# Performance work log

Hardware: AMD Instinct MI355X
Metric: run time of the kernel (lower is better)

Reference implementation:

```python
import jax, jax.numpy as jnp
import numpy as np

N, E, EL = 65536, 1048576, 2097152
IN, H, OUT = 32, 64, 64


def setup_inputs() -> dict:
    key = jax.random.key(0)
    ks = jax.random.split(key, 20)
    inp = {
        "x": jax.random.normal(ks[0], (N, IN), dtype=jnp.float32),
        "edge_index": jax.random.randint(ks[1], (2, E), 0, N, dtype=jnp.int64),
        "edge_weight": jax.random.uniform(ks[2], (E,), dtype=jnp.float32),
        "edge_label_index": jax.random.randint(ks[3], (2, EL), 0, N, dtype=jnp.int64),
    }
    dims = [(IN, H), (H, H), (H, H), (H, H), (H, H), (H, OUT)]
    for i, (di, do) in enumerate(dims):
        scale = (2.0 / (di + do)) ** 0.5
        inp[f"w{i+1}"] = jax.random.normal(ks[4 + i], (di, do), dtype=jnp.float32) * scale
        inp[f"b{i+1}"] = jnp.zeros((do,), dtype=jnp.float32)
    return inp


def _gcn_norm(edge_index, edge_weight, num_nodes):
    # PyG GCNConv default: add self-loops (weight 1), symmetric normalization
    src, dst = edge_index[0], edge_index[1]
    loop = jnp.arange(num_nodes, dtype=edge_index.dtype)
    src_f = jnp.concatenate([src, loop])
    dst_f = jnp.concatenate([dst, loop])
    w_f = jnp.concatenate([edge_weight, jnp.ones((num_nodes,), edge_weight.dtype)])
    deg = jax.ops.segment_sum(w_f, dst_f, num_segments=num_nodes)
    dinv = jnp.where(deg > 0, jax.lax.rsqrt(jnp.where(deg > 0, deg, 1.0)), 0.0)
    norm = dinv[src_f] * w_f * dinv[dst_f]  # [E+N]
    return src_f, dst_f, norm


def _gcn_layer(x, W, b, src_f, dst_f, norm, num_nodes):
    h = x @ W  # transform first, then propagate (PyG GCNConv order)
    msg = norm[:, None] * h[src_f]  # gather + scale along edges
    out = jax.ops.segment_sum(msg, dst_f, num_segments=num_nodes)  # scatter-add
    return out + b


def reference(x, edge_index, edge_weight, edge_label_index,
              w1, b1, w2, b2, w3, b3, w4, b4, w5, b5, w6, b6):
    num_nodes = x.shape[0]
    src_f, dst_f, norm = _gcn_norm(edge_index, edge_weight, num_nodes)
    h = x
    for W, b in [(w1, b1), (w2, b2), (w3, b3), (w4, b4), (w5, b5)]:
        h = jax.nn.relu(_gcn_layer(h, W, b, src_f, dst_f, norm, num_nodes))
        # dropout = identity in deterministic reference
    encoded = _gcn_layer(h, w6, b6, src_f, dst_f, norm, num_nodes)
    # decode: elementwise dot over labeled edge pairs
    decoded = (encoded[edge_label_index[0]] * encoded[edge_label_index[1]]).sum(axis=1)
    return decoded
```

## Files before the change

kernel.cpp:

```cpp
#include <hip/hip_runtime.h>
#include <hip/hip_fp16.h>

#define N_NODES 65536
#define N_EDGES 1048576
#define N_LABEL 2097152
#define DIM_IN 32
#define DIM_H 64

typedef short short8 __attribute__((ext_vector_type(8)));
typedef float floatx4 __attribute__((ext_vector_type(4)));


__global__ void k_init(float* __restrict__ deg, int* __restrict__ cnt) {
    int v = blockIdx.x * blockDim.x + threadIdx.x;
    deg[v] = 1.0f;
    cnt[v] = 0;
}

__global__ void k_cnt(const int* __restrict__ ei, const float* __restrict__ w,
                      int* __restrict__ cnt, float* __restrict__ deg) {
    int e = blockIdx.x * blockDim.x + threadIdx.x;
    int d = ei[N_EDGES + e];
    atomicAdd(&cnt[d], 1);
    atomicAdd(&deg[d], w[e]);
}

__global__ void k_scan1(const int* __restrict__ cnt, int* __restrict__ blksum) {
    int tid = threadIdx.x;
    const int4* p = (const int4*)(cnt + blockIdx.x * 1024);
    int4 v = p[tid];
    int s = v.x + v.y + v.z + v.w;
    for (int d = 1; d < 64; d <<= 1) s += __shfl_xor(s, d);
    __shared__ int wsum[4];
    if ((tid & 63) == 0) wsum[tid >> 6] = s;
    __syncthreads();
    if (tid == 0) blksum[blockIdx.x] = wsum[0] + wsum[1] + wsum[2] + wsum[3];
}

__global__ void k_scan2(int* __restrict__ blksum) {
    if (threadIdx.x == 0) {
        int run = 0;
        for (int i = 0; i < 64; ++i) { int t = blksum[i]; blksum[i] = run; run += t; }
    }
}

__global__ void k_scan3(const int* __restrict__ cnt, const int* __restrict__ blksum,
                        int* __restrict__ offs, int* __restrict__ cursor) {
    int tid = threadIdx.x, bid = blockIdx.x;
    const int4* p = (const int4*)(cnt + bid * 1024);
    int4 v = p[tid];
    int s = v.x + v.y + v.z + v.w;
    int lane = tid & 63, wid = tid >> 6;
    int sc = s;
    for (int d = 1; d < 64; d <<= 1) {
        int t = __shfl_up(sc, d);
        if (lane >= d) sc += t;
    }
    __shared__ int wsum[4];
    if (lane == 63) wsum[wid] = sc;
    __syncthreads();
    int base = blksum[bid];
    for (int w2 = 0; w2 < wid; ++w2) base += wsum[w2];
    int ex = base + sc - s;
    int idx = bid * 1024 + tid * 4;
    int o0 = ex, o1 = o0 + v.x, o2 = o1 + v.y, o3 = o2 + v.z;
    offs[idx] = o0; offs[idx + 1] = o1; offs[idx + 2] = o2; offs[idx + 3] = o3;
    cursor[idx] = o0; cursor[idx + 1] = o1; cursor[idx + 2] = o2; cursor[idx + 3] = o3;
    if (bid == 63 && tid == 255) offs[N_NODES] = o3 + v.w;
}

__global__ void k_dinv(float* __restrict__ deg) {
    int v = blockIdx.x * blockDim.x + threadIdx.x;
    deg[v] = rsqrtf(deg[v]);
}

__global__ void k_fill(const int* __restrict__ ei, const float* __restrict__ w,
                       const float* __restrict__ dinv, int* __restrict__ cursor,
                       int2* __restrict__ csr_se) {
    int e = blockIdx.x * blockDim.x + threadIdx.x;
    int s = ei[e];
    int d = ei[N_EDGES + e];
    int pos = atomicAdd(&cursor[d], 1);
    float nm = dinv[s] * w[e] * dinv[d];
    csr_se[pos] = make_int2(s, __float_as_int(nm));
}


__global__ void k_cast_x(const float* __restrict__ x, __half* __restrict__ xh) {
    int gid = blockIdx.x * 256 + threadIdx.x;
    xh[gid] = __float2half(x[gid]);
}


template <int K>
__global__ void __launch_bounds__(256) k_agg(
        const int* __restrict__ offs, const int2* __restrict__ csr_se,
        const __half* __restrict__ h, const float* __restrict__ dinv,
        float* __restrict__ agg) {
    constexpr int LPE = K / 8;
    constexpr int EPI = 64 / LPE;

    int tid = threadIdx.x;
    int v = blockIdx.x * 4 + (tid >> 6);
    int lane = tid & 63;
    int sub = lane % LPE;
    int g   = lane / LPE;

    float a[8] = {0.f, 0.f, 0.f, 0.f, 0.f, 0.f, 0.f, 0.f};

    if (g == 0) {
        float dv = dinv[v];
        float sl = dv * dv;
        uint4 rv = *(const uint4*)(h + (size_t)v * K + sub * 8);
        const __half2* hp = (const __half2*)&rv;
#pragma unroll
        for (int i = 0; i < 4; ++i) {
            float2 f = __half22float2(hp[i]);
            a[2 * i]     += sl * f.x;
            a[2 * i + 1] += sl * f.y;
        }
    }

    int j0 = __builtin_amdgcn_readfirstlane(offs[v]);
    int j1 = __builtin_amdgcn_readfirstlane(offs[v + 1]);

    for (int jm = j0; jm < j1; jm += 64) {
        int mi = jm + lane;
        int2 md = csr_se[mi < j1 ? mi : j1 - 1];
        if (mi >= j1) md.y = 0;
        int nwin = j1 - jm;
        if (nwin > 64) nwin = 64;
        for (int t = 0; t * EPI < nwin; ++t) {
            int we = t * EPI + g;
            int src = __shfl(md.x, we);
            float nm = __int_as_float(__shfl(md.y, we));
            uint4 rv = *(const uint4*)(h + (size_t)src * K + sub * 8);
            const __half2* hp = (const __half2*)&rv;
#pragma unroll
            for (int i = 0; i < 4; ++i) {
                float2 f = __half22float2(hp[i]);
                a[2 * i]     += nm * f.x;
                a[2 * i + 1] += nm * f.y;
            }
        }
    }

#pragma unroll
    for (int st = LPE; st < 64; st <<= 1) {
#pragma unroll
        for (int i = 0; i < 8; ++i) a[i] += __shfl_xor(a[i], st);
    }

    if (lane < LPE) {
        float* dst = agg + (size_t)v * K + lane * 8;
        *(float4*)(dst)     = make_float4(a[0], a[1], a[2], a[3]);
        *(float4*)(dst + 4) = make_float4(a[4], a[5], a[6], a[7]);
    }
}


__device__ __forceinline__ unsigned short f32_bf16(float f) {
    unsigned u = __float_as_uint(f);
    unsigned r = u + 0x7FFFu + ((u >> 16) & 1u);
    return (unsigned short)(r >> 16);
}
__device__ __forceinline__ float bf16_f32(unsigned short h) {
    return __uint_as_float(((unsigned)h) << 16);
}

template <int KIN, bool RELU>
__global__ void __launch_bounds__(256) k_gemm_mfma(
        const float* __restrict__ agg, const float* __restrict__ W,
        const float* __restrict__ b, __half* __restrict__ out) {
    constexpr int KC = KIN / 32;
    constexpr int NT = N_NODES / 16;
    __shared__ float Wl[KIN * 64];
    int tid = threadIdx.x;
    for (int i = tid; i < KIN * 64; i += 256) Wl[i] = W[i];
    __syncthreads();

    int lane = tid & 63;
    int l15 = lane & 15, l4 = lane >> 4;

    short8 whi[4][KC], wlo[4][KC];
#pragma unroll
    for (int ct = 0; ct < 4; ++ct)
#pragma unroll
        for (int kc = 0; kc < KC; ++kc)
#pragma unroll
            for (int j = 0; j < 8; ++j) {
                float wv = Wl[(kc * 32 + l4 * 8 + j) * 64 + ct * 16 + l15];
                unsigned short hi = f32_bf16(wv);
                unsigned short lo = f32_bf16(wv - bf16_f32(hi));
                whi[ct][kc][j] = (short)hi;
                wlo[ct][kc][j] = (short)lo;
            }
    float bias[4];
#pragma unroll
    for (int ct = 0; ct < 4; ++ct) bias[ct] = b[ct * 16 + l15];

    int wave_id = blockIdx.x * 4 + (tid >> 6);
    for (int tile = wave_id; tile < NT; tile += 2048) {
        int r0 = tile * 16;
        const float* arow = agg + (size_t)(r0 + l15) * KIN + l4 * 8;
        short8 ahi[KC], alo[KC];
#pragma unroll
        for (int kc = 0; kc < KC; ++kc) {
            float4 f0 = *(const float4*)(arow + kc * 32);
            float4 f1 = *(const float4*)(arow + kc * 32 + 4);
            float fv[8] = {f0.x, f0.y, f0.z, f0.w, f1.x, f1.y, f1.z, f1.w};
#pragma unroll
            for (int j = 0; j < 8; ++j) {
                unsigned short hi = f32_bf16(fv[j]);
                unsigned short lo = f32_bf16(fv[j] - bf16_f32(hi));
                ahi[kc][j] = (short)hi;
                alo[kc][j] = (short)lo;
            }
        }
        floatx4 acc[4] = {{0.f,0.f,0.f,0.f},{0.f,0.f,0.f,0.f},{0.f,0.f,0.f,0.f},{0.f,0.f,0.f,0.f}};
#pragma unroll
        for (int ct = 0; ct < 4; ++ct)
#pragma unroll
            for (int kc = 0; kc < KC; ++kc) {
                acc[ct] = __builtin_amdgcn_mfma_f32_16x16x32_bf16(ahi[kc], whi[ct][kc], acc[ct], 0, 0, 0);
                acc[ct] = __builtin_amdgcn_mfma_f32_16x16x32_bf16(ahi[kc], wlo[ct][kc], acc[ct], 0, 0, 0);
                acc[ct] = __builtin_amdgcn_mfma_f32_16x16x32_bf16(alo[kc], whi[ct][kc], acc[ct], 0, 0, 0);
            }
#pragma unroll
        for (int ct = 0; ct < 4; ++ct)
#pragma unroll
            for (int r = 0; r < 4; ++r) {
                float o = acc[ct][r] + bias[ct];
                if (RELU) o = fmaxf(o, 0.f);
                out[(size_t)(r0 + l4 * 4 + r) * 64 + ct * 16 + l15] = __float2half(o);
            }
    }
}


__device__ __forceinline__ float dot8h(uint4 ua, uint4 ub) {
    const __half2* pa = (const __half2*)&ua;
    const __half2* pb = (const __half2*)&ub;
    float s = 0.f;
#pragma unroll
    for (int i = 0; i < 4; ++i) {
        float2 fa = __half22float2(pa[i]);
        float2 fb = __half22float2(pb[i]);
        s += fa.x * fb.x + fa.y * fb.y;
    }
    return s;
}

__global__ void __launch_bounds__(256) k_decode(
        const int* __restrict__ eli, const __half* __restrict__ enc,
        float* __restrict__ out) {
    int gid = blockIdx.x * 256 + threadIdx.x;
    int p = gid >> 3;
    int c8 = gid & 7;
    int a = eli[p];
    int b = eli[N_LABEL + p];
    uint4 ua = *(const uint4*)(enc + (size_t)a * 64 + c8 * 8);
    uint4 ub = *(const uint4*)(enc + (size_t)b * 64 + c8 * 8);
    float s = dot8h(ua, ub);
    s += __shfl_xor(s, 1, 8);
    s += __shfl_xor(s, 2, 8);
    s += __shfl_xor(s, 4, 8);
    if (c8 == 0) out[p] = s;
}


extern "C" void kernel_launch(void* const* d_in, const int* in_sizes, int n_in,
                              void* d_out, int out_size, void* d_ws, size_t ws_size,
                              hipStream_t stream) {
    const float* x   = (const float*)d_in[0];
    const int*   ei  = (const int*)d_in[1];
    const float* ew  = (const float*)d_in[2];
    const int*   eli = (const int*)d_in[3];
    const float* W[6] = {(const float*)d_in[4],  (const float*)d_in[6],
                         (const float*)d_in[8],  (const float*)d_in[10],
                         (const float*)d_in[12], (const float*)d_in[14]};
    const float* B[6] = {(const float*)d_in[5],  (const float*)d_in[7],
                         (const float*)d_in[9],  (const float*)d_in[11],
                         (const float*)d_in[13], (const float*)d_in[15]};

    char* ws = (char*)d_ws;
    float*  dinv    = (float*)ws;   ws += N_NODES * 4;
    int*    cnt     = (int*)ws;     ws += N_NODES * 4;
    int*    offs    = (int*)ws;     ws += (N_NODES + 16) * 4;
    int*    cursor  = (int*)ws;     ws += N_NODES * 4;
    int*    blksum  = (int*)ws;     ws += 256 * 4;
    int2*   csr_se  = (int2*)ws;    ws += (size_t)N_EDGES * 8;
    __half* xh      = (__half*)ws;  ws += (size_t)N_NODES * DIM_IN * 2;
    float*  aggF    = (float*)ws;   ws += (size_t)N_NODES * 64 * 4;
    __half* hA      = (__half*)ws;  ws += (size_t)N_NODES * 64 * 2;
    __half* hB      = (__half*)ws;

    const int BS = 256;
    const int gAgg = N_NODES / 4;
    const int gGemm = 512;

    k_init <<<N_NODES / BS, BS, 0, stream>>>(dinv, cnt);
    k_cnt  <<<N_EDGES / BS, BS, 0, stream>>>(ei, ew, cnt, dinv);
    k_scan1<<<64, BS, 0, stream>>>(cnt, blksum);
    k_scan2<<<1, 64, 0, stream>>>(blksum);
    k_scan3<<<64, BS, 0, stream>>>(cnt, blksum, offs, cursor);
    k_dinv <<<N_NODES / BS, BS, 0, stream>>>(dinv);
    k_fill <<<N_EDGES / BS, BS, 0, stream>>>(ei, ew, dinv, cursor, csr_se);

    k_cast_x<<<N_NODES * DIM_IN / BS, BS, 0, stream>>>(x, xh);

    k_agg<DIM_IN><<<gAgg, BS, 0, stream>>>(offs, csr_se, xh, dinv, aggF);
    k_gemm_mfma<DIM_IN, true><<<gGemm, BS, 0, stream>>>(aggF, W[0], B[0], hA);

    k_agg<DIM_H><<<gAgg, BS, 0, stream>>>(offs, csr_se, hA, dinv, aggF);
    k_gemm_mfma<DIM_H, true><<<gGemm, BS, 0, stream>>>(aggF, W[1], B[1], hB);
    k_agg<DIM_H><<<gAgg, BS, 0, stream>>>(offs, csr_se, hB, dinv, aggF);
    k_gemm_mfma<DIM_H, true><<<gGemm, BS, 0, stream>>>(aggF, W[2], B[2], hA);
    k_agg<DIM_H><<<gAgg, BS, 0, stream>>>(offs, csr_se, hA, dinv, aggF);
    k_gemm_mfma<DIM_H, true><<<gGemm, BS, 0, stream>>>(aggF, W[3], B[3], hB);
    k_agg<DIM_H><<<gAgg, BS, 0, stream>>>(offs, csr_se, hB, dinv, aggF);
    k_gemm_mfma<DIM_H, true><<<gGemm, BS, 0, stream>>>(aggF, W[4], B[4], hA);

    k_agg<DIM_H><<<gAgg, BS, 0, stream>>>(offs, csr_se, hA, dinv, aggF);
    k_gemm_mfma<DIM_H, false><<<gGemm, BS, 0, stream>>>(aggF, W[5], B[5], hB);

    k_decode<<<N_LABEL * 8 / BS, BS, 0, stream>>>(eli, hB, (float*)d_out);
}
```

Before: 490.1 us.

## Pack degree and count into one 64-bit atomic and record per-edge rank

The separate count and float-degree atomics are merged into a single 64-bit atomicAdd: the count sits in the high word and a 2^24 fixed-point weight sum in the low word. The returned old count is stored as each edge's rank, so the CSR fill computes its position as offs[d]+rank[e] and no longer needs a cursor array or a second round of atomics. This halves the atomic traffic in the degree pass and removes atomics from the fill pass. In exchange it adds a 16-bit rank array, makes the degree a fixed-point sum with small rounding error, and relies on per-node degree staying below 65536 and the weight sum fitting in 32 bits.

```diff
diff --git a/kernel.cpp b/kernel.cpp
--- a/kernel.cpp
+++ b/kernel.cpp
@@ -11,25 +11,25 @@
 typedef float floatx4 __attribute__((ext_vector_type(4)));
 
 
-__global__ void k_init(float* __restrict__ deg, int* __restrict__ cnt) {
+__global__ void k_init(unsigned long long* __restrict__ packed) {
     int v = blockIdx.x * blockDim.x + threadIdx.x;
-    deg[v] = 1.0f;
-    cnt[v] = 0;
+    packed[v] = 0ull;
 }
 
 __global__ void k_cnt(const int* __restrict__ ei, const float* __restrict__ w,
-                      int* __restrict__ cnt, float* __restrict__ deg) {
+                      unsigned long long* __restrict__ packed,
+                      unsigned short* __restrict__ rank) {
     int e = blockIdx.x * blockDim.x + threadIdx.x;
     int d = ei[N_EDGES + e];
-    atomicAdd(&cnt[d], 1);
-    atomicAdd(&deg[d], w[e]);
-}
-
-__global__ void k_scan1(const int* __restrict__ cnt, int* __restrict__ blksum) {
+    unsigned fx = __float2uint_rn(w[e] * 16777216.f);
+    unsigned long long old = atomicAdd(&packed[d], (1ull << 32) | (unsigned long long)fx);
+    rank[e] = (unsigned short)(old >> 32);
+}
+
+__global__ void k_scan1(const int2* __restrict__ packed, int* __restrict__ blksum) {
     int tid = threadIdx.x;
-    const int4* p = (const int4*)(cnt + blockIdx.x * 1024);
-    int4 v = p[tid];
-    int s = v.x + v.y + v.z + v.w;
+    const int2* p = packed + blockIdx.x * 1024 + tid * 4;
+    int s = p[0].y + p[1].y + p[2].y + p[3].y;
     for (int d = 1; d < 64; d <<= 1) s += __shfl_xor(s, d);
     __shared__ int wsum[4];
     if ((tid & 63) == 0) wsum[tid >> 6] = s;
@@ -44,12 +44,12 @@
     }
 }
 
-__global__ void k_scan3(const int* __restrict__ cnt, const int* __restrict__ blksum,
-                        int* __restrict__ offs, int* __restrict__ cursor) {
+__global__ void k_scan3(const int2* __restrict__ packed, const int* __restrict__ blksum,
+                        int* __restrict__ offs) {
     int tid = threadIdx.x, bid = blockIdx.x;
-    const int4* p = (const int4*)(cnt + bid * 1024);
-    int4 v = p[tid];
-    int s = v.x + v.y + v.z + v.w;
+    const int2* p = packed + bid * 1024 + tid * 4;
+    int c0 = p[0].y, c1 = p[1].y, c2 = p[2].y, c3 = p[3].y;
+    int s = c0 + c1 + c2 + c3;
     int lane = tid & 63, wid = tid >> 6;
     int sc = s;
     for (int d = 1; d < 64; d <<= 1) {
@@ -63,24 +63,24 @@
     for (int w2 = 0; w2 < wid; ++w2) base += wsum[w2];
     int ex = base + sc - s;
     int idx = bid * 1024 + tid * 4;
-    int o0 = ex, o1 = o0 + v.x, o2 = o1 + v.y, o3 = o2 + v.z;
+    int o0 = ex, o1 = o0 + c0, o2 = o1 + c1, o3 = o2 + c2;
     offs[idx] = o0; offs[idx + 1] = o1; offs[idx + 2] = o2; offs[idx + 3] = o3;
-    cursor[idx] = o0; cursor[idx + 1] = o1; cursor[idx + 2] = o2; cursor[idx + 3] = o3;
-    if (bid == 63 && tid == 255) offs[N_NODES] = o3 + v.w;
-}
-
-__global__ void k_dinv(float* __restrict__ deg) {
+    if (bid == 63 && tid == 255) offs[N_NODES] = o3 + c3;
+}
+
+__global__ void k_dinv(const uint2* __restrict__ packed, float* __restrict__ dinv) {
     int v = blockIdx.x * blockDim.x + threadIdx.x;
-    deg[v] = rsqrtf(deg[v]);
+    float deg = 1.0f + (float)packed[v].x * (1.f / 16777216.f);
+    dinv[v] = rsqrtf(deg);
 }
 
 __global__ void k_fill(const int* __restrict__ ei, const float* __restrict__ w,
-                       const float* __restrict__ dinv, int* __restrict__ cursor,
-                       int2* __restrict__ csr_se) {
+                       const float* __restrict__ dinv, const int* __restrict__ offs,
+                       const unsigned short* __restrict__ rank, int2* __restrict__ csr_se) {
     int e = blockIdx.x * blockDim.x + threadIdx.x;
     int s = ei[e];
     int d = ei[N_EDGES + e];
-    int pos = atomicAdd(&cursor[d], 1);
+    int pos = offs[d] + rank[e];
     float nm = dinv[s] * w[e] * dinv[d];
     csr_se[pos] = make_int2(s, __float_as_int(nm));
 }
@@ -284,28 +284,28 @@
                          (const float*)d_in[13], (const float*)d_in[15]};
 
     char* ws = (char*)d_ws;
-    float*  dinv    = (float*)ws;   ws += N_NODES * 4;
-    int*    cnt     = (int*)ws;     ws += N_NODES * 4;
-    int*    offs    = (int*)ws;     ws += (N_NODES + 16) * 4;
-    int*    cursor  = (int*)ws;     ws += N_NODES * 4;
-    int*    blksum  = (int*)ws;     ws += 256 * 4;
-    int2*   csr_se  = (int2*)ws;    ws += (size_t)N_EDGES * 8;
-    __half* xh      = (__half*)ws;  ws += (size_t)N_NODES * DIM_IN * 2;
-    float*  aggF    = (float*)ws;   ws += (size_t)N_NODES * 64 * 4;
-    __half* hA      = (__half*)ws;  ws += (size_t)N_NODES * 64 * 2;
-    __half* hB      = (__half*)ws;
+    unsigned long long* packed = (unsigned long long*)ws;  ws += (size_t)N_NODES * 8;
+    float*          dinv    = (float*)ws;           ws += N_NODES * 4;
+    int*            offs    = (int*)ws;             ws += (N_NODES + 16) * 4;
+    int*            blksum  = (int*)ws;             ws += 256 * 4;
+    unsigned short* rank    = (unsigned short*)ws;  ws += (size_t)N_EDGES * 2;
+    int2*           csr_se  = (int2*)ws;            ws += (size_t)N_EDGES * 8;
+    __half*         xh      = (__half*)ws;          ws += (size_t)N_NODES * DIM_IN * 2;
+    float*          aggF    = (float*)ws;           ws += (size_t)N_NODES * 64 * 4;
+    __half*         hA      = (__half*)ws;          ws += (size_t)N_NODES * 64 * 2;
+    __half*         hB      = (__half*)ws;
 
     const int BS = 256;
     const int gAgg = N_NODES / 4;
     const int gGemm = 512;
 
-    k_init <<<N_NODES / BS, BS, 0, stream>>>(dinv, cnt);
-    k_cnt  <<<N_EDGES / BS, BS, 0, stream>>>(ei, ew, cnt, dinv);
-    k_scan1<<<64, BS, 0, stream>>>(cnt, blksum);
+    k_init <<<N_NODES / BS, BS, 0, stream>>>(packed);
+    k_cnt  <<<N_EDGES / BS, BS, 0, stream>>>(ei, ew, packed, rank);
+    k_scan1<<<64, BS, 0, stream>>>((const int2*)packed, blksum);
     k_scan2<<<1, 64, 0, stream>>>(blksum);
-    k_scan3<<<64, BS, 0, stream>>>(cnt, blksum, offs, cursor);
-    k_dinv <<<N_NODES / BS, BS, 0, stream>>>(dinv);
-    k_fill <<<N_EDGES / BS, BS, 0, stream>>>(ei, ew, dinv, cursor, csr_se);
+    k_scan3<<<64, BS, 0, stream>>>((const int2*)packed, blksum, offs);
+    k_dinv <<<N_NODES / BS, BS, 0, stream>>>((const uint2*)packed, dinv);
+    k_fill <<<N_EDGES / BS, BS, 0, stream>>>(ei, ew, dinv, offs, rank, csr_se);
 
     k_cast_x<<<N_NODES * DIM_IN / BS, BS, 0, stream>>>(x, xh);
 
```

New measurement: 413.6 us. 15.6% less time.
